# Performance work log

Measured on AMD Instinct MI355X. Metric: run time of the kernel, lower is better.

Reference implementation:

```python
import jax, jax.numpy as jnp
import numpy as np

N_NODES = 100000
N_EDGES = 1600000
IN_C, HID_C, OUT_C = 128, 64, 40
BN_EPS = 1e-5


def setup_inputs() -> dict:
    key = jax.random.key(0)
    ks = jax.random.split(key, 12)
    def lin(k, fan_in, fan_out):
        bound = 1.0 / np.sqrt(fan_in)
        return jax.random.uniform(k, (fan_in, fan_out), jnp.float32, -bound, bound)
    x = jax.random.normal(ks[0], (N_NODES, IN_C), jnp.float32)
    edge_index = jax.random.randint(ks[1], (2, N_EDGES), 0, N_NODES, jnp.int64)
    return {
        "x": x,
        "edge_index": edge_index,
        "W1": lin(ks[2], IN_C, HID_C), "b1": jnp.zeros((HID_C,), jnp.float32),
        "g1": jnp.ones((HID_C,), jnp.float32), "be1": jnp.zeros((HID_C,), jnp.float32),
        "W2": lin(ks[3], HID_C, HID_C), "b2": jnp.zeros((HID_C,), jnp.float32),
        "g2": jnp.ones((HID_C,), jnp.float32), "be2": jnp.zeros((HID_C,), jnp.float32),
        "W3": lin(ks[4], HID_C, OUT_C), "b3": jnp.zeros((OUT_C,), jnp.float32),
    }


def _gcn_conv(h, W, b, src, dst, edge_norm, self_norm):
    # linear transform then symmetric-normalized aggregation (GCN with self loops)
    h = h @ W + b
    msg = h[src] * edge_norm[:, None]                      # [E, C] gather
    agg = jax.ops.segment_sum(msg, dst, num_segments=N_NODES)  # scatter-add
    return agg + h * self_norm[:, None]


def _bn_relu(h, gamma, beta):
    mu = jnp.mean(h, axis=0)
    var = jnp.mean(jnp.square(h - mu), axis=0)
    return jax.nn.relu((h - mu) * jax.lax.rsqrt(var + BN_EPS) * gamma + beta)


def reference(x, edge_index, W1, b1, g1, be1, W2, b2, g2, be2, W3, b3):
    src, dst = edge_index[0], edge_index[1]
    # degree with self loops (computed on dst, as in PyG GCNConv)
    deg = jax.ops.segment_sum(jnp.ones((N_EDGES,), x.dtype), dst,
                              num_segments=N_NODES) + 1.0
    dis = jax.lax.rsqrt(deg)
    edge_norm = dis[src] * dis[dst]   # [E]
    self_norm = 1.0 / deg             # [N]

    h = _gcn_conv(x, W1, b1, src, dst, edge_norm, self_norm)
    h = _bn_relu(h, g1, be1)
    h = _gcn_conv(h, W2, b2, src, dst, edge_norm, self_norm)
    h = _bn_relu(h, g2, be2)
    h = _gcn_conv(h, W3, b3, src, dst, edge_norm, self_norm)
    return h
```

## Files before the change

kernel.cpp:

```cpp
#include <hip/hip_runtime.h>

#define N_NODES 100000
#define N_EDGES 1600000
#define NBKT 391
#define EPB 4096
#define NBLK_E ((N_EDGES + EPB - 1) / EPB)

typedef unsigned short u16;
typedef unsigned int u32;
struct alignas(8) bf4 { u16 a, b, c, d; };

__device__ __forceinline__ float blo(u32 u) { return __uint_as_float(u << 16); }
__device__ __forceinline__ float bhi(u32 u) { return __uint_as_float(u & 0xffff0000u); }
__device__ __forceinline__ u16 f2bf(float f) {
  u32 u = __float_as_uint(f);
  return (u16)((u + 0x7fffu + ((u >> 16) & 1u)) >> 16);
}


__global__ __launch_bounds__(256) void bucket_count_k(const int* __restrict__ dst,
                                                      int* __restrict__ gCount) {
  __shared__ int h[NBKT];
  for (int i = threadIdx.x; i < NBKT; i += 256) h[i] = 0;
  __syncthreads();
  const int e0 = blockIdx.x * EPB;
  const int eN = min(EPB, N_EDGES - e0);
  for (int i = threadIdx.x; i < eN; i += 256) atomicAdd(&h[dst[e0 + i] >> 8], 1);
  __syncthreads();
  for (int i = threadIdx.x; i < NBKT; i += 256)
    if (h[i]) atomicAdd(&gCount[i], h[i]);
}

__global__ void bucket_scan_k(const int* __restrict__ gCount,
                              int* __restrict__ gBase,
                              int* __restrict__ gCursor,
                              int* __restrict__ offsets) {
  __shared__ int sm[512];
  const int t = threadIdx.x;
  const int c0 = (t < NBKT) ? gCount[t] : 0;
  const int c1 = (t + 256 < NBKT) ? gCount[t + 256] : 0;
  sm[t] = c0; sm[t + 256] = c1;
  __syncthreads();
  for (int off = 1; off < 512; off <<= 1) {
    const int v0 = (t >= off) ? sm[t - off] : 0;
    const int v1 = (t + 256 >= off) ? sm[t + 256 - off] : 0;
    __syncthreads();
    sm[t] += v0; sm[t + 256] += v1;
    __syncthreads();
  }
  if (t < NBKT)       { const int b = sm[t] - c0;       gBase[t] = b;       gCursor[t] = b; }
  if (t + 256 < NBKT) { const int b = sm[t + 256] - c1; gBase[t + 256] = b; gCursor[t + 256] = b; }
  if (t == 0) { gBase[NBKT] = N_EDGES; offsets[N_NODES] = N_EDGES; }
}

__global__ __launch_bounds__(256) void bucket_scatter_k(const int* __restrict__ src,
                                                        const int* __restrict__ dst,
                                                        int* __restrict__ gCursor,
                                                        uint2* __restrict__ ebuf) {
  __shared__ int cnt[NBKT];
  __shared__ int inc[512];
  __shared__ int gb[NBKT];
  __shared__ int cur[NBKT];
  __shared__ uint2 st[EPB];
  const int t = threadIdx.x;
  for (int i = t; i < NBKT; i += 256) cnt[i] = 0;
  __syncthreads();
  const int e0 = blockIdx.x * EPB;
  const int eN = min(EPB, N_EDGES - e0);
  for (int i = t; i < eN; i += 256) atomicAdd(&cnt[dst[e0 + i] >> 8], 1);
  __syncthreads();
  const int c0 = (t < NBKT) ? cnt[t] : 0;
  const int c1 = (t + 256 < NBKT) ? cnt[t + 256] : 0;
  inc[t] = c0; inc[t + 256] = c1;
  __syncthreads();
  for (int off = 1; off < 512; off <<= 1) {
    const int v0 = (t >= off) ? inc[t - off] : 0;
    const int v1 = (t + 256 >= off) ? inc[t + 256 - off] : 0;
    __syncthreads();
    inc[t] += v0; inc[t + 256] += v1;
    __syncthreads();
  }
  if (t < NBKT) {
    if (c0) gb[t] = atomicAdd(&gCursor[t], c0);
    cur[t] = inc[t] - c0;
  }
  if (t + 256 < NBKT) {
    if (c1) gb[t + 256] = atomicAdd(&gCursor[t + 256], c1);
    cur[t + 256] = inc[t + 256] - c1;
  }
  __syncthreads();
  for (int i = t; i < eN; i += 256) {
    const int d = dst[e0 + i];
    const int b = d >> 8;
    const int p = atomicAdd(&cur[b], 1);
    st[p] = make_uint2((unsigned)src[e0 + i], (unsigned)d);
  }
  __syncthreads();
  for (int i = t; i < eN; i += 256) {
    const uint2 e = st[i];
    const int b = (int)(e.y >> 8);
    const int excl = inc[b] - cnt[b];
    ebuf[gb[b] + (i - excl)] = e;
  }
}

__global__ __launch_bounds__(256) void csr_build_k(const uint2* __restrict__ ebuf,
                                                   const int* __restrict__ gBase,
                                                   int* __restrict__ offsets,
                                                   int* __restrict__ csr_src,
                                                   float* __restrict__ dis,
                                                   float* __restrict__ selfn) {
  __shared__ int cnt[256];
  __shared__ int inc[256];
  __shared__ int cur[256];
  const int t = threadIdx.x;
  const int b = blockIdx.x;
  const int ebeg = gBase[b], eend = gBase[b + 1];
  cnt[t] = 0;
  __syncthreads();
  for (int e = ebeg + t; e < eend; e += 256) atomicAdd(&cnt[ebuf[e].y & 255], 1);
  __syncthreads();
  const int c = cnt[t];
  inc[t] = c;
  __syncthreads();
  for (int off = 1; off < 256; off <<= 1) {
    const int v = (t >= off) ? inc[t - off] : 0;
    __syncthreads();
    inc[t] += v;
    __syncthreads();
  }
  const int node = (b << 8) + t;
  const int goff = ebeg + inc[t] - c;
  cur[t] = goff;
  if (node < N_NODES) {
    offsets[node] = goff;
    const float deg = (float)c + 1.0f;
    dis[node] = rsqrtf(deg);
    selfn[node] = 1.0f / deg;
  }
  __syncthreads();
  for (int e = ebeg + t; e < eend; e += 256) {
    const uint2 ed = ebuf[e];
    const int p = atomicAdd(&cur[ed.y & 255], 1);
    csr_src[p] = (int)ed.x;
  }
}

__global__ __launch_bounds__(256) void pack_k(const int* __restrict__ csr_src,
                                              const float* __restrict__ dis,
                                              int2* __restrict__ csr2) {
  const int i = blockIdx.x * 256 + threadIdx.x;
  if (i < N_EDGES) {
    const int v = csr_src[i] & 0xFFFFF;
    csr2[i] = make_int2(v, __float_as_int(dis[v]));
  }
}


template <int K, int C, int RPT, bool BN>
__global__ __launch_bounds__(256) void gemm_k(const float* __restrict__ A,
                                              const float* __restrict__ W,
                                              const float* __restrict__ bias,
                                              const float* __restrict__ scale,
                                              const float* __restrict__ shift,
                                              u16* __restrict__ out) {
  constexpr int CQ = C / 4;
  constexpr int TR = 256 / CQ;
  constexpr int ROWS = TR * RPT;
  __shared__ __align__(16) float Wl[K * C];
  __shared__ __align__(16) float Al[ROWS * K];
  const int tid = threadIdx.x;
  for (int i = tid; i < K * C; i += 256) Wl[i] = W[i];
  const int row0 = blockIdx.x * ROWS;
  for (int i = tid; i < ROWS * K; i += 256) {
    int r = i / K, k = i - r * K;
    int gr = row0 + r;
    float v = 0.f;
    if (gr < N_NODES) {
      v = A[(size_t)gr * K + k];
      if (BN) v = fmaxf(fmaf(v, scale[k], shift[k]), 0.f);
    }
    Al[i] = v;
  }
  __syncthreads();
  const int cq = tid % CQ;
  const int rs = tid / CQ;
  if (rs >= TR) return;
  const float4* W4 = (const float4*)Wl;
  const float4* A4 = (const float4*)Al;
  float4 acc[RPT];
#pragma unroll
  for (int i = 0; i < RPT; ++i) acc[i] = make_float4(0.f, 0.f, 0.f, 0.f);
#pragma unroll 4
  for (int k4 = 0; k4 < K / 4; ++k4) {
    float4 w0 = W4[(4 * k4 + 0) * CQ + cq];
    float4 w1 = W4[(4 * k4 + 1) * CQ + cq];
    float4 w2 = W4[(4 * k4 + 2) * CQ + cq];
    float4 w3 = W4[(4 * k4 + 3) * CQ + cq];
#pragma unroll
    for (int i = 0; i < RPT; ++i) {
      float4 a = A4[(rs * RPT + i) * (K / 4) + k4];
      acc[i].x = fmaf(a.x, w0.x, acc[i].x); acc[i].y = fmaf(a.x, w0.y, acc[i].y);
      acc[i].z = fmaf(a.x, w0.z, acc[i].z); acc[i].w = fmaf(a.x, w0.w, acc[i].w);
      acc[i].x = fmaf(a.y, w1.x, acc[i].x); acc[i].y = fmaf(a.y, w1.y, acc[i].y);
      acc[i].z = fmaf(a.y, w1.z, acc[i].z); acc[i].w = fmaf(a.y, w1.w, acc[i].w);
      acc[i].x = fmaf(a.z, w2.x, acc[i].x); acc[i].y = fmaf(a.z, w2.y, acc[i].y);
      acc[i].z = fmaf(a.z, w2.z, acc[i].z); acc[i].w = fmaf(a.z, w2.w, acc[i].w);
      acc[i].x = fmaf(a.w, w3.x, acc[i].x); acc[i].y = fmaf(a.w, w3.y, acc[i].y);
      acc[i].z = fmaf(a.w, w3.z, acc[i].z); acc[i].w = fmaf(a.w, w3.w, acc[i].w);
    }
  }
  float4 b4 = ((const float4*)bias)[cq];
#pragma unroll
  for (int i = 0; i < RPT; ++i) {
    int gr = row0 + rs * RPT + i;
    if (gr < N_NODES) {
      bf4 o;
      o.a = f2bf(acc[i].x + b4.x); o.b = f2bf(acc[i].y + b4.y);
      o.c = f2bf(acc[i].z + b4.z); o.d = f2bf(acc[i].w + b4.w);
      *(bf4*)(out + (size_t)gr * C + cq * 4) = o;
    }
  }
}


template <bool STATS>
__global__ __launch_bounds__(256) void agg64_v3_k(const u16* __restrict__ tb,
                                                  const int2* __restrict__ csr2,
                                                  const int* __restrict__ offs,
                                                  const float* __restrict__ dis,
                                                  const float* __restrict__ selfn,
                                                  float* __restrict__ out,
                                                  float* __restrict__ part) {
  __shared__ float s_sum[64];
  __shared__ float s_sq[64];
  if (STATS) {
    if (threadIdx.x < 64) { s_sum[threadIdx.x] = 0.f; s_sq[threadIdx.x] = 0.f; }
    __syncthreads();
  }
  const int lane = threadIdx.x & 63;
  const int nb = (blockIdx.x * 4 + (threadIdx.x >> 6)) * 4;
  const int g = lane >> 3;
  const int c4 = lane & 7;
  const int i = g >> 1;
  const int p = g & 1;
  const int node = nb + i;
  int beg = 0, end = 0;
  if (node < N_NODES) { beg = offs[node]; end = offs[node + 1]; }
  int iters = (end - beg + 1) >> 1;
  iters = max(iters, __shfl_xor(iters, 8));
  iters = max(iters, __shfl_xor(iters, 16));
  iters = max(iters, __shfl_xor(iters, 32));
  float acc[8];
#pragma unroll
  for (int k = 0; k < 8; ++k) acc[k] = 0.f;
  const u16* __restrict__ tc = tb + (c4 << 3);
  int e = beg + p;
#pragma unroll 4
  for (int it = 0; it < iters; ++it) {
    int2 ev = make_int2(0, 0);
    if (e < end) ev = csr2[e];
    e += 2;
    const int s = ev.x & 0xFFFFF;
    const float w = __int_as_float(ev.y);
    const uint4 q = *(const uint4*)(tc + (size_t)s * 64);
    acc[0] = fmaf(blo(q.x), w, acc[0]);
    acc[1] = fmaf(bhi(q.x), w, acc[1]);
    acc[2] = fmaf(blo(q.y), w, acc[2]);
    acc[3] = fmaf(bhi(q.y), w, acc[3]);
    acc[4] = fmaf(blo(q.z), w, acc[4]);
    acc[5] = fmaf(bhi(q.z), w, acc[5]);
    acc[6] = fmaf(blo(q.w), w, acc[6]);
    acc[7] = fmaf(bhi(q.w), w, acc[7]);
  }
#pragma unroll
  for (int k = 0; k < 8; ++k) acc[k] += __shfl_xor(acc[k], 8);
  float v[8];
  const bool writer = (p == 0) && (node < N_NODES);
  if (writer) {
    const float dn = dis[node], sn = selfn[node];
    const uint4 q = *(const uint4*)(tb + (size_t)node * 64 + (c4 << 3));
    const float sv[8] = {blo(q.x), bhi(q.x), blo(q.y), bhi(q.y),
                         blo(q.z), bhi(q.z), blo(q.w), bhi(q.w)};
#pragma unroll
    for (int k = 0; k < 8; ++k) v[k] = fmaf(dn, acc[k], sv[k] * sn);
    float4* op = (float4*)(out + (size_t)node * 64 + (c4 << 3));
    op[0] = make_float4(v[0], v[1], v[2], v[3]);
    op[1] = make_float4(v[4], v[5], v[6], v[7]);
  }
  if (STATS) {
    if (writer) {
#pragma unroll
      for (int k = 0; k < 8; ++k) {
        atomicAdd(&s_sum[(c4 << 3) + k], v[k]);
        atomicAdd(&s_sq[(c4 << 3) + k], v[k] * v[k]);
      }
    }
    __syncthreads();
    if (threadIdx.x < 128) {
      const int c = threadIdx.x & 63;
      const float val = (threadIdx.x < 64) ? s_sum[c] : s_sq[c];
      atomicAdd(&part[(blockIdx.x & 63) * 128 + (threadIdx.x < 64 ? c : 64 + c)], val);
    }
  }
}

__global__ __launch_bounds__(256) void agg40_v3_k(const u16* __restrict__ tb,
                                                  const int2* __restrict__ csr2,
                                                  const int* __restrict__ offs,
                                                  const float* __restrict__ dis,
                                                  const float* __restrict__ selfn,
                                                  float* __restrict__ out) {
  const int lane = threadIdx.x & 63;
  const int nb = (blockIdx.x * 4 + (threadIdx.x >> 6)) * 4;
  const bool ok = lane < 60;
  const int g = ok ? (lane / 5) : 0;
  const int c4 = ok ? (lane - g * 5) : 0;
  const int i = g / 3;
  const int p = g - i * 3;
  const int node = nb + i;
  int beg = 0, end = 0;
  if (ok && node < N_NODES) { beg = offs[node]; end = offs[node + 1]; }
  int iters = (end - beg + 2) / 3;
  iters = max(iters, __shfl_xor(iters, 1));
  iters = max(iters, __shfl_xor(iters, 2));
  iters = max(iters, __shfl_xor(iters, 4));
  iters = max(iters, __shfl_xor(iters, 8));
  iters = max(iters, __shfl_xor(iters, 16));
  iters = max(iters, __shfl_xor(iters, 32));
  float acc[8];
#pragma unroll
  for (int k = 0; k < 8; ++k) acc[k] = 0.f;
  const u16* __restrict__ tc = tb + (c4 << 3);
  int e = beg + p;
#pragma unroll 4
  for (int it = 0; it < iters; ++it) {
    int2 ev = make_int2(0, 0);
    if (e < end) ev = csr2[e];
    e += 3;
    const int s = ev.x & 0xFFFFF;
    const float w = __int_as_float(ev.y);
    const uint4 q = *(const uint4*)(tc + (size_t)s * 40);
    acc[0] = fmaf(blo(q.x), w, acc[0]);
    acc[1] = fmaf(bhi(q.x), w, acc[1]);
    acc[2] = fmaf(blo(q.y), w, acc[2]);
    acc[3] = fmaf(bhi(q.y), w, acc[3]);
    acc[4] = fmaf(blo(q.z), w, acc[4]);
    acc[5] = fmaf(bhi(q.z), w, acc[5]);
    acc[6] = fmaf(blo(q.w), w, acc[6]);
    acc[7] = fmaf(bhi(q.w), w, acc[7]);
  }
  const int base = 15 * i + c4;
  float tot[8];
#pragma unroll
  for (int k = 0; k < 8; ++k) {
    tot[k] = __shfl(acc[k], base) + __shfl(acc[k], base + 5) + __shfl(acc[k], base + 10);
  }
  if (ok && p == 0 && node < N_NODES) {
    const float dn = dis[node], sn = selfn[node];
    const uint4 q = *(const uint4*)(tb + (size_t)node * 40 + (c4 << 3));
    const float sv[8] = {blo(q.x), bhi(q.x), blo(q.y), bhi(q.y),
                         blo(q.z), bhi(q.z), blo(q.w), bhi(q.w)};
    float v[8];
#pragma unroll
    for (int k = 0; k < 8; ++k) v[k] = fmaf(dn, tot[k], sv[k] * sn);
    float4* op = (float4*)(out + (size_t)node * 40 + (c4 << 3));
    op[0] = make_float4(v[0], v[1], v[2], v[3]);
    op[1] = make_float4(v[4], v[5], v[6], v[7]);
  }
}

__global__ void bnfinal_k(const float* __restrict__ part, const float* __restrict__ g,
                          const float* __restrict__ be, float* __restrict__ scale,
                          float* __restrict__ shift) {
  const int c = threadIdx.x;
  float s = 0.f, q = 0.f;
  for (int b = 0; b < 64; ++b) { s += part[b * 128 + c]; q += part[b * 128 + 64 + c]; }
  const float inv = 1.0f / (float)N_NODES;
  const float mu = s * inv;
  const float var = q * inv - mu * mu;
  const float sc = g[c] * rsqrtf(var + 1e-5f);
  scale[c] = sc;
  shift[c] = fmaf(-mu, sc, be[c]);
}


extern "C" void kernel_launch(void* const* d_in, const int* in_sizes, int n_in,
                              void* d_out, int out_size, void* d_ws, size_t ws_size,
                              hipStream_t stream) {
  const float* x   = (const float*)d_in[0];
  const int*   ei  = (const int*)d_in[1];
  const float* W1  = (const float*)d_in[2];
  const float* b1  = (const float*)d_in[3];
  const float* g1  = (const float*)d_in[4];
  const float* be1 = (const float*)d_in[5];
  const float* W2  = (const float*)d_in[6];
  const float* b2  = (const float*)d_in[7];
  const float* g2  = (const float*)d_in[8];
  const float* be2 = (const float*)d_in[9];
  const float* W3  = (const float*)d_in[10];
  const float* b3  = (const float*)d_in[11];
  float* out = (float*)d_out;
  const int* src = ei;
  const int* dst = ei + N_EDGES;

  char* ws = (char*)d_ws;
  size_t o = 0;
  auto alloc = [&](size_t bytes) -> char* {
    char* p = ws + o;
    o += (bytes + 255) & ~(size_t)255;
    return p;
  };
  int*   gCount  = (int*)alloc((size_t)NBKT * 4);
  int*   gBase   = (int*)alloc(((size_t)NBKT + 1) * 4);
  int*   gCursor = (int*)alloc((size_t)NBKT * 4);
  int*   offsets = (int*)alloc(((size_t)N_NODES + 1) * 4);
  int*   csr_src = (int*)alloc((size_t)N_EDGES * 4);
  float* dis     = (float*)alloc((size_t)N_NODES * 4);
  float* selfn   = (float*)alloc((size_t)N_NODES * 4);
  float* part1   = (float*)alloc(64 * 128 * 4);
  float* part2   = (float*)alloc(64 * 128 * 4);
  float* scale1  = (float*)alloc(64 * 4);
  float* shift1  = (float*)alloc(64 * 4);
  float* scale2  = (float*)alloc(64 * 4);
  float* shift2  = (float*)alloc(64 * 4);
  char*  treg    = alloc((size_t)N_NODES * 64 * 4);
  float* hbuf    = (float*)alloc((size_t)N_NODES * 64 * 4);
  u16*  tbuf = (u16*)treg;
  uint2* ebuf = (uint2*)treg;
  int2* csr2 = (int2*)(treg + (size_t)N_NODES * 64 * 2);

  hipMemsetAsync(gCount, 0, (size_t)NBKT * 4, stream);
  hipMemsetAsync(part1, 0, 2 * 64 * 128 * 4, stream);

  bucket_count_k<<<NBLK_E, 256, 0, stream>>>(dst, gCount);
  bucket_scan_k<<<1, 256, 0, stream>>>(gCount, gBase, gCursor, offsets);
  bucket_scatter_k<<<NBLK_E, 256, 0, stream>>>(src, dst, gCursor, ebuf);
  csr_build_k<<<NBKT, 256, 0, stream>>>(ebuf, gBase, offsets, csr_src, dis, selfn);
  pack_k<<<(N_EDGES + 255) / 256, 256, 0, stream>>>(csr_src, dis, csr2);

  const int nagg = (N_NODES + 15) / 16;

  gemm_k<128, 64, 2, false><<<(N_NODES + 31) / 32, 256, 0, stream>>>(
      x, W1, b1, nullptr, nullptr, tbuf);
  agg64_v3_k<true><<<nagg, 256, 0, stream>>>(
      tbuf, csr2, offsets, dis, selfn, hbuf, part1);
  bnfinal_k<<<1, 64, 0, stream>>>(part1, g1, be1, scale1, shift1);

  gemm_k<64, 64, 4, true><<<(N_NODES + 63) / 64, 256, 0, stream>>>(
      hbuf, W2, b2, scale1, shift1, tbuf);
  agg64_v3_k<true><<<nagg, 256, 0, stream>>>(
      tbuf, csr2, offsets, dis, selfn, hbuf, part2);
  bnfinal_k<<<1, 64, 0, stream>>>(part2, g2, be2, scale2, shift2);

  gemm_k<64, 40, 4, true><<<(N_NODES + 99) / 100, 256, 0, stream>>>(
      hbuf, W3, b3, scale2, shift2, tbuf);
  agg40_v3_k<<<nagg, 256, 0, stream>>>(
      tbuf, csr2, offsets, dis, selfn, out);
}
```

Before: 528.4 us.

## Store aggregated hidden activations in bf16 and vectorize GEMM input staging

The 64-wide aggregation kernels now write their output as packed bf16 instead of fp32, and the following GEMMs read that bf16 buffer. This halves the bytes for the hidden buffer write and read. The GEMM A-tile loader now moves four elements per load and applies the BN scale/shift in vector form. Neighbor gathers in both aggregation kernels use nontemporal loads. The BN statistics are still computed from the fp32 values, but the next layer consumes bf16-rounded activations, which adds rounding error.

```diff
diff --git a/kernel.cpp b/kernel.cpp
--- a/kernel.cpp
+++ b/kernel.cpp
@@ -8,6 +8,7 @@
 
 typedef unsigned short u16;
 typedef unsigned int u32;
+typedef u32 u32x4 __attribute__((ext_vector_type(4)));
 struct alignas(8) bf4 { u16 a, b, c, d; };
 
 __device__ __forceinline__ float blo(u32 u) { return __uint_as_float(u << 16); }
@@ -15,6 +16,9 @@
 __device__ __forceinline__ u16 f2bf(float f) {
   u32 u = __float_as_uint(f);
   return (u16)((u + 0x7fffu + ((u >> 16) & 1u)) >> 16);
+}
+__device__ __forceinline__ u32 pack2(float a, float b) {
+  return (u32)f2bf(a) | ((u32)f2bf(b) << 16);
 }
 
 
@@ -157,8 +161,8 @@
 }
 
 
-template <int K, int C, int RPT, bool BN>
-__global__ __launch_bounds__(256) void gemm_k(const float* __restrict__ A,
+template <int K, int C, int RPT, bool BN, bool BF16IN>
+__global__ __launch_bounds__(256) void gemm_k(const void* __restrict__ Av,
                                               const float* __restrict__ W,
                                               const float* __restrict__ bias,
                                               const float* __restrict__ scale,
@@ -172,15 +176,29 @@
   const int tid = threadIdx.x;
   for (int i = tid; i < K * C; i += 256) Wl[i] = W[i];
   const int row0 = blockIdx.x * ROWS;
-  for (int i = tid; i < ROWS * K; i += 256) {
-    int r = i / K, k = i - r * K;
-    int gr = row0 + r;
-    float v = 0.f;
+  for (int i = tid; i < ROWS * K / 4; i += 256) {
+    const int e0 = i * 4;
+    const int r = e0 / K, k = e0 - (e0 / K) * K;
+    const int gr = row0 + r;
+    float v0 = 0.f, v1 = 0.f, v2 = 0.f, v3 = 0.f;
     if (gr < N_NODES) {
-      v = A[(size_t)gr * K + k];
-      if (BN) v = fmaxf(fmaf(v, scale[k], shift[k]), 0.f);
+      if (BF16IN) {
+        const uint2 u = *(const uint2*)((const u16*)Av + (size_t)gr * K + k);
+        v0 = blo(u.x); v1 = bhi(u.x); v2 = blo(u.y); v3 = bhi(u.y);
+      } else {
+        const float4 a = *(const float4*)((const float*)Av + (size_t)gr * K + k);
+        v0 = a.x; v1 = a.y; v2 = a.z; v3 = a.w;
+      }
+      if (BN) {
+        const float4 sc = *(const float4*)(scale + k);
+        const float4 sh = *(const float4*)(shift + k);
+        v0 = fmaxf(fmaf(v0, sc.x, sh.x), 0.f);
+        v1 = fmaxf(fmaf(v1, sc.y, sh.y), 0.f);
+        v2 = fmaxf(fmaf(v2, sc.z, sh.z), 0.f);
+        v3 = fmaxf(fmaf(v3, sc.w, sh.w), 0.f);
+      }
     }
-    Al[i] = v;
+    *(float4*)(Al + r * K + k) = make_float4(v0, v1, v2, v3);
   }
   __syncthreads();
   const int cq = tid % CQ;
@@ -225,12 +243,12 @@
 
 
 template <bool STATS>
-__global__ __launch_bounds__(256) void agg64_v3_k(const u16* __restrict__ tb,
+__global__ __launch_bounds__(256) void agg64_v4_k(const u16* __restrict__ tb,
                                                   const int2* __restrict__ csr2,
                                                   const int* __restrict__ offs,
                                                   const float* __restrict__ dis,
                                                   const float* __restrict__ selfn,
-                                                  float* __restrict__ out,
+                                                  u16* __restrict__ out,
                                                   float* __restrict__ part) {
   __shared__ float s_sum[64];
   __shared__ float s_sq[64];
@@ -263,7 +281,7 @@
     e += 2;
     const int s = ev.x & 0xFFFFF;
     const float w = __int_as_float(ev.y);
-    const uint4 q = *(const uint4*)(tc + (size_t)s * 64);
+    const u32x4 q = __builtin_nontemporal_load((const u32x4*)(tc + (size_t)s * 64));
     acc[0] = fmaf(blo(q.x), w, acc[0]);
     acc[1] = fmaf(bhi(q.x), w, acc[1]);
     acc[2] = fmaf(blo(q.y), w, acc[2]);
@@ -284,9 +302,10 @@
                          blo(q.z), bhi(q.z), blo(q.w), bhi(q.w)};
 #pragma unroll
     for (int k = 0; k < 8; ++k) v[k] = fmaf(dn, acc[k], sv[k] * sn);
-    float4* op = (float4*)(out + (size_t)node * 64 + (c4 << 3));
-    op[0] = make_float4(v[0], v[1], v[2], v[3]);
-    op[1] = make_float4(v[4], v[5], v[6], v[7]);
+    uint4 o;
+    o.x = pack2(v[0], v[1]); o.y = pack2(v[2], v[3]);
+    o.z = pack2(v[4], v[5]); o.w = pack2(v[6], v[7]);
+    *(uint4*)(out + (size_t)node * 64 + (c4 << 3)) = o;
   }
   if (STATS) {
     if (writer) {
@@ -305,7 +324,7 @@
   }
 }
 
-__global__ __launch_bounds__(256) void agg40_v3_k(const u16* __restrict__ tb,
+__global__ __launch_bounds__(256) void agg40_v4_k(const u16* __restrict__ tb,
                                                   const int2* __restrict__ csr2,
                                                   const int* __restrict__ offs,
                                                   const float* __restrict__ dis,
@@ -340,7 +359,7 @@
     e += 3;
     const int s = ev.x & 0xFFFFF;
     const float w = __int_as_float(ev.y);
-    const uint4 q = *(const uint4*)(tc + (size_t)s * 40);
+    const u32x4 q = __builtin_nontemporal_load((const u32x4*)(tc + (size_t)s * 40));
     acc[0] = fmaf(blo(q.x), w, acc[0]);
     acc[1] = fmaf(bhi(q.x), w, acc[1]);
     acc[2] = fmaf(blo(q.y), w, acc[2]);
@@ -425,7 +444,7 @@
   float* scale2  = (float*)alloc(64 * 4);
   float* shift2  = (float*)alloc(64 * 4);
   char*  treg    = alloc((size_t)N_NODES * 64 * 4);
-  float* hbuf    = (float*)alloc((size_t)N_NODES * 64 * 4);
+  u16*   hbuf    = (u16*)alloc((size_t)N_NODES * 64 * 2);
   u16*  tbuf = (u16*)treg;
   uint2* ebuf = (uint2*)treg;
   int2* csr2 = (int2*)(treg + (size_t)N_NODES * 64 * 2);
@@ -441,20 +460,20 @@
 
   const int nagg = (N_NODES + 15) / 16;
 
-  gemm_k<128, 64, 2, false><<<(N_NODES + 31) / 32, 256, 0, stream>>>(
+  gemm_k<128, 64, 2, false, false><<<(N_NODES + 31) / 32, 256, 0, stream>>>(
       x, W1, b1, nullptr, nullptr, tbuf);
-  agg64_v3_k<true><<<nagg, 256, 0, stream>>>(
+  agg64_v4_k<true><<<nagg, 256, 0, stream>>>(
       tbuf, csr2, offsets, dis, selfn, hbuf, part1);
   bnfinal_k<<<1, 64, 0, stream>>>(part1, g1, be1, scale1, shift1);
 
-  gemm_k<64, 64, 4, true><<<(N_NODES + 63) / 64, 256, 0, stream>>>(
+  gemm_k<64, 64, 4, true, true><<<(N_NODES + 63) / 64, 256, 0, stream>>>(
       hbuf, W2, b2, scale1, shift1, tbuf);
-  agg64_v3_k<true><<<nagg, 256, 0, stream>>>(
+  agg64_v4_k<true><<<nagg, 256, 0, stream>>>(
       tbuf, csr2, offsets, dis, selfn, hbuf, part2);
   bnfinal_k<<<1, 64, 0, stream>>>(part2, g2, be2, scale2, shift2);
 
-  gemm_k<64, 40, 4, true><<<(N_NODES + 99) / 100, 256, 0, stream>>>(
+  gemm_k<64, 40, 4, true, true><<<(N_NODES + 99) / 100, 256, 0, stream>>>(
       hbuf, W3, b3, scale2, shift2, tbuf);
-  agg40_v3_k<<<nagg, 256, 0, stream>>>(
+  agg40_v4_k<<<nagg, 256, 0, stream>>>(
       tbuf, csr2, offsets, dis, selfn, out);
 }
```

New measurement: 539.7 us. +2.1%, slower.
